# Performance work log

Hardware: AMD Instinct MI355X
Metric: run time of the kernel (lower is better)

## Reference

```python
import jax, jax.numpy as jnp
import numpy as np

NUM_HEADS = 16
NUM_GQA_GROUPS = 4
HEAD_DIM = 128
TOTAL_TOKENS = 4096
NUM_SEQS = 8
SCALE = HEAD_DIM ** -0.5


def setup_inputs() -> dict:
    key = jax.random.key(0)
    kq, kk, kv, kc = jax.random.split(key, 4)
    query = jax.random.normal(kq, (TOTAL_TOKENS, NUM_HEADS, HEAD_DIM), dtype=jnp.float32)
    k = jax.random.normal(kk, (TOTAL_TOKENS, NUM_GQA_GROUPS, HEAD_DIM), dtype=jnp.float32)
    v = jax.random.normal(kv, (TOTAL_TOKENS, NUM_GQA_GROUPS, HEAD_DIM), dtype=jnp.float32)
    # cu_seqlens: sorted prefix boundaries, pinned to 0 and TOTAL_TOKENS
    inner = jnp.sort(jax.random.randint(kc, (NUM_SEQS - 1,), 1, TOTAL_TOKENS, dtype=jnp.int32))
    cu_seqlens = jnp.concatenate([
        jnp.zeros((1,), jnp.int32), inner,
        jnp.full((1,), TOTAL_TOKENS, jnp.int32)])
    return {"query": query, "key": k, "value": v, "cu_seqlens": cu_seqlens}


def reference(query, key, value, cu_seqlens):
    """Packed varlen (thd) causal attention with GQA, fused via a segment mask.

    query: [T, H, D]; key/value: [T, G, D]; cu_seqlens: [B+1] int32.
    Returns [T, H, D] (same layout the torch thd path concatenates back to).
    """
    T, H, D = query.shape
    ratio = H // key.shape[1]
    if ratio > 1:  # GQA: repeat kv heads to match query heads
        key = jnp.repeat(key, ratio, axis=1)
        value = jnp.repeat(value, ratio, axis=1)

    pos = jnp.arange(T, dtype=jnp.int32)
    # segment id of each packed token: cu[j] <= i < cu[j+1]
    seg = jnp.searchsorted(cu_seqlens, pos, side="right") - 1
    # within-segment causal mask (global causal == local causal inside a segment)
    mask = (seg[:, None] == seg[None, :]) & (pos[:, None] >= pos[None, :])  # [T, T]

    scores = jnp.einsum("qhd,khd->hqk", query, key) * SCALE  # [H, T, T]
    scores = jnp.where(mask[None], scores, -jnp.inf)
    probs = jax.nn.softmax(scores, axis=-1)
    out = jnp.einsum("hqk,khd->qhd", probs, value)  # [T, H, D]
    return out
```

## Files before the change

### kernel.cpp

```cpp
#include <hip/hip_runtime.h>
#include <hip/hip_bf16.h>


#define T_TOK 4096
#define NH    16
#define NG    4
#define HD    128
#define NCU   9

typedef short          short8_t __attribute__((ext_vector_type(8)));
typedef float          float4_t __attribute__((ext_vector_type(4)));
typedef unsigned int   uint2_t  __attribute__((ext_vector_type(2)));
typedef unsigned short ushort;

static __device__ inline unsigned pack2(float a, float b) {
    __hip_bfloat162 h = __float22bfloat162_rn(make_float2(a, b));
    union { __hip_bfloat162 h; unsigned u; } c; c.h = h;
    return c.u;
}
static __device__ inline short8_t cvt8(float4_t lo, float4_t hi) {
    union { unsigned u[4]; short8_t s; } r;
    r.u[0] = pack2(lo[0], lo[1]); r.u[1] = pack2(lo[2], lo[3]);
    r.u[2] = pack2(hi[0], hi[1]); r.u[3] = pack2(hi[2], hi[3]);
    return r.s;
}

__global__ __launch_bounds__(512) void attn_fwd(
    const float* __restrict__ Q,
    const float* __restrict__ K,
    const float* __restrict__ V,
    const int*   __restrict__ cu,
    float*       __restrict__ O)
{
    __shared__ __align__(16) unsigned char smem[58368];
    ushort (*Ks)[32][136]   = (ushort (*)[32][136])smem;
    ushort (*Vt)[128][40]   = (ushort (*)[128][40])(smem + 17408);
    ushort (*pb)[2][16][40] = (ushort (*)[2][16][40])(smem + 37888);

    const int qtile = (int)gridDim.x - 1 - (int)blockIdx.x;
    const int g     = blockIdx.y;
    const int tid   = threadIdx.x;
    const int wave  = tid >> 6;
    const int split = wave >> 2;
    const int hw    = wave & 3;
    const int lane  = tid & 63;
    const int h     = g * 4 + hw;
    const int col   = lane & 15;
    const int quad  = lane >> 4;

    const int qbase = qtile * 32;
    const int qq[2] = { qbase + col, qbase + 16 + col };

    int seg_start[2] = {0, 0}, seg0 = 0;
    #pragma unroll
    for (int j = 1; j < NCU; ++j) {
        int cj = cu[j];
        if (cj <= qq[0])  seg_start[0] = cj;
        if (cj <= qq[1])  seg_start[1] = cj;
        if (cj <= qbase)  seg0         = cj;
    }
    const int k0   = seg0 & ~31;
    const int nblk = (qbase + 32 - k0) >> 5;
    const int nb0  = (nblk + 1) >> 1;
    const int kstart = k0 + split * nb0 * 32;

    short8_t qf[2][4];
    #pragma unroll
    for (int tt = 0; tt < 2; ++tt) {
        const float* qp = Q + ((long)qq[tt] * NH + h) * HD + quad * 8;
        #pragma unroll
        for (int c = 0; c < 4; ++c)
            qf[tt][c] = cvt8(*(const float4_t*)(qp + c * 32),
                             *(const float4_t*)(qp + c * 32 + 4));
    }

    float4_t oacc[2][8];
    #pragma unroll
    for (int tt = 0; tt < 2; ++tt)
        #pragma unroll
        for (int dt = 0; dt < 8; ++dt) oacc[tt][dt] = (float4_t){0.f, 0.f, 0.f, 0.f};

    float m_run[2] = {-10000.0f, -10000.0f};
    float l_run[2] = {0.0f, 0.0f};
    const float c_scale = 0.08838834764831845f * 1.4426950408889634f;

    const int stid = tid & 255;
    const int ki  = stid >> 3;
    const int ch  = (stid & 7) * 16;
    const int kp2 = (stid & 15) * 2;
    const int dc  = (stid >> 4) * 8;

    float4_t kreg[4], vreg[4];
    {
        int key = kstart + ki; if (key > T_TOK - 1) key = T_TOK - 1;
        const float* kp = K + ((long)key * NG + g) * HD + ch;
        kreg[0] = *(const float4_t*)kp;       kreg[1] = *(const float4_t*)(kp + 4);
        kreg[2] = *(const float4_t*)(kp + 8); kreg[3] = *(const float4_t*)(kp + 12);
        int key0 = kstart + kp2;     if (key0 > T_TOK - 1) key0 = T_TOK - 1;
        int key1 = kstart + kp2 + 1; if (key1 > T_TOK - 1) key1 = T_TOK - 1;
        const float* v0 = V + ((long)key0 * NG + g) * HD + dc;
        const float* v1 = V + ((long)key1 * NG + g) * HD + dc;
        vreg[0] = *(const float4_t*)v0; vreg[1] = *(const float4_t*)(v0 + 4);
        vreg[2] = *(const float4_t*)v1; vreg[3] = *(const float4_t*)(v1 + 4);
    }

    for (int it = 0; it < nb0; ++it) {
        const int kb = kstart + it * 32;
        __syncthreads();

        *(short8_t*)&Ks[split][ki][ch]     = cvt8(kreg[0], kreg[1]);
        *(short8_t*)&Ks[split][ki][ch + 8] = cvt8(kreg[2], kreg[3]);
        #pragma unroll
        for (int d = 0; d < 4; ++d) {
            *(unsigned*)&Vt[split][dc + d][kp2]     = pack2(vreg[0][d], vreg[2][d]);
            *(unsigned*)&Vt[split][dc + 4 + d][kp2] = pack2(vreg[1][d], vreg[3][d]);
        }
        __syncthreads();

        {
            int nb = kb + 32;
            int key = nb + ki; if (key > T_TOK - 1) key = T_TOK - 1;
            const float* kp = K + ((long)key * NG + g) * HD + ch;
            kreg[0] = *(const float4_t*)kp;       kreg[1] = *(const float4_t*)(kp + 4);
            kreg[2] = *(const float4_t*)(kp + 8); kreg[3] = *(const float4_t*)(kp + 12);
            int key0 = nb + kp2;     if (key0 > T_TOK - 1) key0 = T_TOK - 1;
            int key1 = nb + kp2 + 1; if (key1 > T_TOK - 1) key1 = T_TOK - 1;
            const float* v0 = V + ((long)key0 * NG + g) * HD + dc;
            const float* v1 = V + ((long)key1 * NG + g) * HD + dc;
            vreg[0] = *(const float4_t*)v0; vreg[1] = *(const float4_t*)(v0 + 4);
            vreg[2] = *(const float4_t*)v1; vreg[3] = *(const float4_t*)(v1 + 4);
        }

        float4_t st[2][2];
        #pragma unroll
        for (int tt = 0; tt < 2; ++tt)
            #pragma unroll
            for (int t = 0; t < 2; ++t) st[tt][t] = (float4_t){0.f, 0.f, 0.f, 0.f};
        #pragma unroll
        for (int c = 0; c < 4; ++c) {
            short8_t kf0 = *(const short8_t*)&Ks[split][col][c * 32 + quad * 8];
            short8_t kf1 = *(const short8_t*)&Ks[split][16 + col][c * 32 + quad * 8];
            st[0][0] = __builtin_amdgcn_mfma_f32_16x16x32_bf16(kf0, qf[0][c], st[0][0], 0, 0, 0);
            st[0][1] = __builtin_amdgcn_mfma_f32_16x16x32_bf16(kf1, qf[0][c], st[0][1], 0, 0, 0);
            st[1][0] = __builtin_amdgcn_mfma_f32_16x16x32_bf16(kf0, qf[1][c], st[1][0], 0, 0, 0);
            st[1][1] = __builtin_amdgcn_mfma_f32_16x16x32_bf16(kf1, qf[1][c], st[1][1], 0, 0, 0);
        }

        #pragma unroll
        for (int tt = 0; tt < 2; ++tt) {
            float tv[8];
            #pragma unroll
            for (int t = 0; t < 2; ++t)
                #pragma unroll
                for (int r = 0; r < 4; ++r) {
                    int key = kb + 16 * t + quad * 4 + r;
                    bool valid = (key <= qq[tt]) && (key >= seg_start[tt]);
                    tv[t * 4 + r] = valid ? st[tt][t][r] * c_scale : -30000.0f;
                }
            float tmax = tv[0];
            #pragma unroll
            for (int i = 1; i < 8; ++i) tmax = fmaxf(tmax, tv[i]);
            tmax = fmaxf(tmax, __shfl_xor(tmax, 16));
            tmax = fmaxf(tmax, __shfl_xor(tmax, 32));
            const float m_new = fmaxf(m_run[tt], tmax);
            const float alpha = __builtin_exp2f(m_run[tt] - m_new);
            float p[8], ps = 0.f;
            #pragma unroll
            for (int i = 0; i < 8; ++i) { p[i] = __builtin_exp2f(tv[i] - m_new); ps += p[i]; }
            ps += __shfl_xor(ps, 16);
            ps += __shfl_xor(ps, 32);
            l_run[tt] = l_run[tt] * alpha + ps;
            m_run[tt] = m_new;
            #pragma unroll
            for (int dt = 0; dt < 8; ++dt) oacc[tt][dt] *= alpha;

            uint2_t w0; w0.x = pack2(p[0], p[1]); w0.y = pack2(p[2], p[3]);
            uint2_t w1; w1.x = pack2(p[4], p[5]); w1.y = pack2(p[6], p[7]);
            *(uint2_t*)&pb[wave][tt][col][quad * 4]      = w0;
            *(uint2_t*)&pb[wave][tt][col][16 + quad * 4] = w1;
        }
        short8_t pf0 = *(const short8_t*)&pb[wave][0][col][quad * 8];
        short8_t pf1 = *(const short8_t*)&pb[wave][1][col][quad * 8];

        #pragma unroll
        for (int dt = 0; dt < 8; ++dt) {
            short8_t vf = *(const short8_t*)&Vt[split][dt * 16 + col][quad * 8];
            oacc[0][dt] = __builtin_amdgcn_mfma_f32_16x16x32_bf16(vf, pf0, oacc[0][dt], 0, 0, 0);
            oacc[1][dt] = __builtin_amdgcn_mfma_f32_16x16x32_bf16(vf, pf1, oacc[1][dt], 0, 0, 0);
        }
    }

    float* Ob = (float*)smem;
    float* cm = (float*)(smem + 34816);
    float* cl = (float*)(smem + 35840);
    #pragma unroll
    for (int tt = 0; tt < 2; ++tt) {
        __syncthreads();
        if (split == 1) {
            if (quad == 0) { cm[hw * 16 + col] = m_run[tt]; cl[hw * 16 + col] = l_run[tt]; }
            float* ob = Ob + (hw * 16 + col) * 132;
            #pragma unroll
            for (int dt = 0; dt < 8; ++dt)
                *(float4_t*)(ob + dt * 16 + quad * 4) = oacc[tt][dt];
        }
        __syncthreads();
        if (split == 0) {
            const float m1 = cm[hw * 16 + col], l1 = cl[hw * 16 + col];
            const float m  = fmaxf(m_run[tt], m1);
            const float a0 = __builtin_exp2f(m_run[tt] - m);
            const float a1 = __builtin_exp2f(m1 - m);
            const float* ob = Ob + (hw * 16 + col) * 132;
            #pragma unroll
            for (int dt = 0; dt < 8; ++dt) {
                float4_t o1 = *(const float4_t*)(ob + dt * 16 + quad * 4);
                oacc[tt][dt] = oacc[tt][dt] * a0 + o1 * a1;
            }
            l_run[tt] = l_run[tt] * a0 + l1 * a1;
        }
    }

    if (split == 0) {
        #pragma unroll
        for (int tt = 0; tt < 2; ++tt) {
            const float inv_l = 1.0f / l_run[tt];
            float* op = O + ((long)qq[tt] * NH + h) * HD + quad * 4;
            #pragma unroll
            for (int dt = 0; dt < 8; ++dt) {
                float4_t ov;
                #pragma unroll
                for (int r = 0; r < 4; ++r) ov[r] = oacc[tt][dt][r] * inv_l;
                *(float4_t*)(op + dt * 16) = ov;
            }
        }
    }
}

extern "C" void kernel_launch(void* const* d_in, const int* in_sizes, int n_in,
                              void* d_out, int out_size, void* d_ws, size_t ws_size,
                              hipStream_t stream) {
    const float* Q  = (const float*)d_in[0];
    const float* K  = (const float*)d_in[1];
    const float* V  = (const float*)d_in[2];
    const int*   cu = (const int*)d_in[3];
    float*       O  = (float*)d_out;
    dim3 grid(T_TOK / 32, NG);
    attn_fwd<<<grid, 512, 0, stream>>>(Q, K, V, cu, O);
}
```

Measured before the change: 215.2 us.

## Split long KV ranges into chunks across blocks and merge partial results

Adds a split-KV (flash-decoding style) path. Each query tile's key range is cut into chunks of up to 32 key blocks, each processed by its own block along grid z, and a second merge kernel combines the partial outputs using the saved m/l statistics. This is meant to balance work for the long causal tiles and raise parallelism. It also skips the rescale of the running softmax state when no lane's max increased. The cost is an extra launch plus partial outputs written to and read back from workspace, and the path runs only when the workspace is large enough.

Result: no change. 213.9 us (-0.6%).

```diff
diff --git a/kernel.cpp b/kernel.cpp
--- a/kernel.cpp
+++ b/kernel.cpp
@@ -8,6 +8,8 @@
 #define HD    128
 #define NCU   9
 
+#define ML_OFF 33554432l
+
 typedef short          short8_t __attribute__((ext_vector_type(8)));
 typedef float          float4_t __attribute__((ext_vector_type(4)));
 typedef unsigned int   uint2_t  __attribute__((ext_vector_type(2)));
@@ -25,12 +27,14 @@
     return r.s;
 }
 
-__global__ __launch_bounds__(512) void attn_fwd(
+template <bool CHUNKED>
+__global__ __launch_bounds__(512) void attn_fwd_k(
     const float* __restrict__ Q,
     const float* __restrict__ K,
     const float* __restrict__ V,
     const int*   __restrict__ cu,
-    float*       __restrict__ O)
+    float*       __restrict__ O,
+    float*       __restrict__ WS)
 {
     __shared__ __align__(16) unsigned char smem[58368];
     ushort (*Ks)[32][136]   = (ushort (*)[32][136])smem;
@@ -39,6 +43,7 @@
 
     const int qtile = (int)gridDim.x - 1 - (int)blockIdx.x;
     const int g     = blockIdx.y;
+    const int cz    = CHUNKED ? (int)blockIdx.z : 0;
     const int tid   = threadIdx.x;
     const int wave  = tid >> 6;
     const int split = wave >> 2;
@@ -59,10 +64,14 @@
         if (cj <= qq[1])  seg_start[1] = cj;
         if (cj <= qbase)  seg0         = cj;
     }
-    const int k0   = seg0 & ~31;
-    const int nblk = (qbase + 32 - k0) >> 5;
-    const int nb0  = (nblk + 1) >> 1;
-    const int kstart = k0 + split * nb0 * 32;
+    const int k0       = seg0 & ~31;
+    const int nblk_tot = (qbase + 32 - k0) >> 5;
+    const int nc       = CHUNKED ? ((nblk_tot + 31) >> 5) : 1;
+    if (CHUNKED && cz >= nc) return;
+    int nblk = nblk_tot - (cz << 5);
+    if (CHUNKED && nblk > 32) nblk = 32;
+    const int nb0    = (nblk + 1) >> 1;
+    const int kstart = k0 + (cz << 10) + split * nb0 * 32;
 
     short8_t qf[2][4];
     #pragma unroll
@@ -163,16 +172,20 @@
             tmax = fmaxf(tmax, __shfl_xor(tmax, 16));
             tmax = fmaxf(tmax, __shfl_xor(tmax, 32));
             const float m_new = fmaxf(m_run[tt], tmax);
-            const float alpha = __builtin_exp2f(m_run[tt] - m_new);
             float p[8], ps = 0.f;
             #pragma unroll
             for (int i = 0; i < 8; ++i) { p[i] = __builtin_exp2f(tv[i] - m_new); ps += p[i]; }
             ps += __shfl_xor(ps, 16);
             ps += __shfl_xor(ps, 32);
-            l_run[tt] = l_run[tt] * alpha + ps;
-            m_run[tt] = m_new;
-            #pragma unroll
-            for (int dt = 0; dt < 8; ++dt) oacc[tt][dt] *= alpha;
+            if (__any(tmax > m_run[tt])) {
+                const float alpha = __builtin_exp2f(m_run[tt] - m_new);
+                l_run[tt] = l_run[tt] * alpha + ps;
+                m_run[tt] = m_new;
+                #pragma unroll
+                for (int dt = 0; dt < 8; ++dt) oacc[tt][dt] *= alpha;
+            } else {
+                l_run[tt] += ps;
+            }
 
             uint2_t w0; w0.x = pack2(p[0], p[1]); w0.y = pack2(p[2], p[3]);
             uint2_t w1; w1.x = pack2(p[4], p[5]); w1.y = pack2(p[6], p[7]);
@@ -216,23 +229,91 @@
                 oacc[tt][dt] = oacc[tt][dt] * a0 + o1 * a1;
             }
             l_run[tt] = l_run[tt] * a0 + l1 * a1;
+            m_run[tt] = m;
         }
     }
 
     if (split == 0) {
-        #pragma unroll
-        for (int tt = 0; tt < 2; ++tt) {
-            const float inv_l = 1.0f / l_run[tt];
-            float* op = O + ((long)qq[tt] * NH + h) * HD + quad * 4;
-            #pragma unroll
-            for (int dt = 0; dt < 8; ++dt) {
-                float4_t ov;
+        if (!CHUNKED || nc == 1) {
+            #pragma unroll
+            for (int tt = 0; tt < 2; ++tt) {
+                const float inv_l = 1.0f / l_run[tt];
+                float* op = O + ((long)qq[tt] * NH + h) * HD + quad * 4;
                 #pragma unroll
-                for (int r = 0; r < 4; ++r) ov[r] = oacc[tt][dt][r] * inv_l;
-                *(float4_t*)(op + dt * 16) = ov;
+                for (int dt = 0; dt < 8; ++dt) {
+                    float4_t ov;
+                    #pragma unroll
+                    for (int r = 0; r < 4; ++r) ov[r] = oacc[tt][dt][r] * inv_l;
+                    *(float4_t*)(op + dt * 16) = ov;
+                }
             }
-        }
-    }
+        } else {
+            const long slot = ((long)(qtile * 4 + g)) * 4 + cz;
+            #pragma unroll
+            for (int tt = 0; tt < 2; ++tt) {
+                const int ql = tt * 16 + col;
+                if (quad == 0) {
+                    float* mlp = WS + ML_OFF + (slot * 128 + hw * 32 + ql) * 2;
+                    mlp[0] = m_run[tt];
+                    mlp[1] = l_run[tt];
+                }
+                float* op = WS + (slot * 128 + hw * 32 + ql) * 128 + quad * 4;
+                #pragma unroll
+                for (int dt = 0; dt < 8; ++dt)
+                    *(float4_t*)(op + dt * 16) = oacc[tt][dt];
+            }
+        }
+    }
+}
+
+__global__ __launch_bounds__(256) void attn_merge(
+    const int*   __restrict__ cu,
+    const float* __restrict__ WS,
+    float*       __restrict__ O)
+{
+    const int tile  = blockIdx.x;
+    const int g     = blockIdx.y;
+    const int qbase = tile * 32;
+    int seg0 = 0;
+    #pragma unroll
+    for (int j = 1; j < NCU; ++j) { int cj = cu[j]; if (cj <= qbase) seg0 = cj; }
+    const int k0       = seg0 & ~31;
+    const int nblk_tot = (qbase + 32 - k0) >> 5;
+    const int nc       = (nblk_tot + 31) >> 5;
+    if (nc <= 1) return;
+
+    const int tid  = threadIdx.x;
+    const int pair = tid >> 1;
+    const int half = tid & 1;
+    const int hw   = pair >> 5;
+    const int q    = pair & 31;
+
+    float m = -30000.0f, l = 0.0f;
+    float4_t acc[16];
+    #pragma unroll
+    for (int i = 0; i < 16; ++i) acc[i] = (float4_t){0.f, 0.f, 0.f, 0.f};
+
+    for (int c = 0; c < nc; ++c) {
+        const long slot = ((long)(tile * 4 + g)) * 4 + c;
+        const float* mlp = WS + ML_OFF + (slot * 128 + pair) * 2;
+        const float mc = mlp[0], lc = mlp[1];
+        const float mn = fmaxf(m, mc);
+        const float a0 = __builtin_exp2f(m - mn);
+        const float a1 = __builtin_exp2f(mc - mn);
+        l = l * a0 + lc * a1;
+        const float* op = WS + (slot * 128 + pair) * 128 + half * 64;
+        #pragma unroll
+        for (int i = 0; i < 16; ++i) {
+            float4_t v = *(const float4_t*)(op + i * 4);
+            acc[i] = acc[i] * a0 + v * a1;
+        }
+        m = mn;
+    }
+    const float inv = 1.0f / l;
+    float* o = O + ((long)(qbase + q) * NH + g * 4 + hw) * HD + half * 64;
+    #pragma unroll
+    for (int i = 0; i < 16; ++i)
+        *(float4_t*)(o + i * 4) = acc[i] * inv;
 }
 
 extern "C" void kernel_launch(void* const* d_in, const int* in_sizes, int n_in,
@@ -243,6 +324,14 @@
     const float* V  = (const float*)d_in[2];
     const int*   cu = (const int*)d_in[3];
     float*       O  = (float*)d_out;
-    dim3 grid(T_TOK / 32, NG);
-    attn_fwd<<<grid, 512, 0, stream>>>(Q, K, V, cu, O);
-}
+    const size_t need = (size_t)(33554432l + 524288l) * sizeof(float);
+    if (d_ws != nullptr && ws_size >= need) {
+        attn_fwd_k<true><<<dim3(T_TOK / 32, NG, 4), 512, 0, stream>>>(
+            Q, K, V, cu, O, (float*)d_ws);
+        attn_merge<<<dim3(T_TOK / 32, NG), 256, 0, stream>>>(
+            cu, (const float*)d_ws, O);
+    } else {
+        attn_fwd_k<false><<<dim3(T_TOK / 32, NG), 512, 0, stream>>>(
+            Q, K, V, cu, O, nullptr);
+    }
+}
```
